# Kernel tuning notes

Hardware: AMD Instinct MI355X
Metric: run time of the kernel (lower is better)

## Reference

```python
import jax, jax.numpy as jnp
import numpy as np

IMG = 416                      # image_shape
DIST = 1075.0                  # isocenter_distance
N_ANG = 320                    # 360 / rotation_resolution(=1.125 deg)
N_DET = IMG                    # detector bins
N_SAMP = IMG                   # integration samples per ray
SCALE = 512.0 / 416.0 * 0.03   # self.scale


def _ray_coords():
    """Pixel-space sample coordinates for every (angle, detector, sample).
    Returns cols, rows of shape [N_ANG, N_DET, N_SAMP] and the step length dt."""
    thetas = (jnp.arange(N_ANG, dtype=jnp.float32) * np.float32(2.0 * np.pi / N_ANG))
    half_diag = (IMG / 2.0) * np.sqrt(2.0)
    gamma_max = np.float32(np.arcsin(half_diag / DIST))  # half fan angle covering image
    gammas = jnp.linspace(-gamma_max, gamma_max, N_DET, dtype=jnp.float32)
    ray_len = np.float32(IMG * np.sqrt(2.0))             # chord length through image
    ts = jnp.linspace(np.float32(DIST - ray_len / 2.0),
                      np.float32(DIST + ray_len / 2.0), N_SAMP, dtype=jnp.float32)
    dt = float(ray_len / (N_SAMP - 1))

    th = thetas[:, None, None]        # [A,1,1]
    gm = gammas[None, :, None]        # [1,D,1]
    t = ts[None, None, :]             # [1,1,S]
    # source position on circle of radius DIST, ray direction toward detector
    sx = np.float32(DIST) * jnp.cos(th)
    sy = np.float32(DIST) * jnp.sin(th)
    x = sx - t * jnp.cos(th + gm)     # [A,D,S] world coords (isocenter at origin)
    y = sy - t * jnp.sin(th + gm)
    ctr = np.float32((IMG - 1) / 2.0)
    return x + ctr, y + ctr, dt       # pixel (col, row) coordinates


def _bilinear(img, cols, rows):
    """Zero-padded bilinear sampling of img[H,W] at float (row,col) coords."""
    c0 = jnp.floor(cols)
    r0 = jnp.floor(rows)
    wc = cols - c0
    wr = rows - r0
    c0i = c0.astype(jnp.int32)
    r0i = r0.astype(jnp.int32)

    def g(ri, ci):
        inb = (ri >= 0) & (ri < IMG) & (ci >= 0) & (ci < IMG)
        v = img[jnp.clip(ri, 0, IMG - 1), jnp.clip(ci, 0, IMG - 1)]
        return jnp.where(inb, v, jnp.float32(0.0))

    return (g(r0i, c0i) * (1 - wr) * (1 - wc)
            + g(r0i, c0i + 1) * (1 - wr) * wc
            + g(r0i + 1, c0i) * wr * (1 - wc)
            + g(r0i + 1, c0i + 1) * wr * wc)


def fan_beam_fp(vol):
    """vol: [B,H,W] -> sinogram [B, N_ANG, N_DET] via ray integration."""
    cols, rows, dt = _ray_coords()
    proj_one = lambda img: _bilinear(img, cols, rows).sum(axis=-1) * jnp.float32(dt)
    return jax.vmap(proj_one)(vol)


def setup_inputs() -> dict:
    key = jax.random.key(0)
    k1, k2 = jax.random.split(key)
    inp = jax.random.normal(k1, (1, 1, IMG, IMG), dtype=jnp.float32)
    tgt = jax.random.normal(k2, (1, 1, IMG, IMG), dtype=jnp.float32)
    return {"input": inp, "target": tgt}


def reference(input, target):
    input_proj = fan_beam_fp(input[:, 0])   # squeeze(1)
    target_proj = fan_beam_fp(target[:, 0])
    return jnp.mean((input_proj - target_proj) ** 2) * jnp.float32(SCALE)
```

## Files before the change

### kernel.cpp

```cpp
#include <hip/hip_runtime.h>
#include <math.h>

#define IMG 416
#define N_ANG 320
#define N_DET 416
#define N_SAMP 416
#define NK (N_SAMP / 8)

#define PSTRIDE 432
#define PROWS   418
#define PBYTES  ((size_t)PROWS * PSTRIDE * 8)

static __device__ __forceinline__ unsigned int f2bf(float f) {
    unsigned int x = __float_as_uint(f);
    return (x + 0x7fffu + ((x >> 16) & 1u)) >> 16;
}

__global__ __launch_bounds__(256) void pack_kernel(const float* __restrict__ a,
                                                   const float* __restrict__ b,
                                                   uint2* __restrict__ P,
                                                   float* __restrict__ out) {
    int i = blockIdx.x * 256 + threadIdx.x;
    if (i == 0) out[0] = 0.0f;
    if (i >= PROWS * PSTRIDE) return;
    int pr = i / PSTRIDE;
    int pc = i - pr * PSTRIDE;
    int r = pr - 1, c = pc - 1;
    float v00 = 0.f, v01 = 0.f, v10 = 0.f, v11 = 0.f;
    bool c0in = (unsigned)c < (unsigned)IMG;
    bool c1in = (unsigned)(c + 1) < (unsigned)IMG;
    if ((unsigned)r < (unsigned)IMG) {
        int base = r * IMG;
        if (c0in) v00 = a[base + c] - b[base + c];
        if (c1in) v01 = a[base + c + 1] - b[base + c + 1];
    }
    if ((unsigned)(r + 1) < (unsigned)IMG) {
        int base = (r + 1) * IMG;
        if (c0in) v10 = a[base + c] - b[base + c];
        if (c1in) v11 = a[base + c + 1] - b[base + c + 1];
    }
    uint2 u;
    u.x = f2bf(v00) | (f2bf(v01) << 16);
    u.y = f2bf(v10) | (f2bf(v11) << 16);
    P[i] = u;
}

__global__ void zero_out_kernel(float* __restrict__ out) {
    if (threadIdx.x == 0) out[0] = 0.0f;
}

__global__ __launch_bounds__(256) void proj_packed(const uint2* __restrict__ P,
                                                   float* __restrict__ out,
                                                   float theta_step, float gmax,
                                                   float gstep, float t0,
                                                   float dtstep, float coef) {
    const int lane = threadIdx.x & 63;
    const int wave = (blockIdx.x * 256 + threadIdx.x) >> 6;
    const int det_base = wave << 3;
    const int a  = det_base / N_DET;
    const int d  = det_base - a * N_DET + (lane >> 3);
    const int s0 = lane & 7;

    const float theta = (float)a * theta_step;
    const float gamma = fmaf((float)d, gstep, -gmax);
    float s1, c1, s2, c2;
    sincosf(theta, &s1, &c1);
    sincosf(theta + gamma, &s2, &c2);
    const float sx = fmaf(1075.0f, c1, 207.5f);
    const float sy = fmaf(1075.0f, s1, 207.5f);

    const float dt8 = 8.0f * dtstep;
    const float tstart = fmaf((float)s0, dtstep, t0);

    const float c2g = (fabsf(c2) < 1e-12f) ? 1e-12f : c2;
    const float s2g = (fabsf(s2) < 1e-12f) ? 1e-12f : s2;
    const float ix = 1.0f / c2g, iy = 1.0f / s2g;
    const float tax = (sx - 416.5f) * ix, tbx = (sx + 1.5f) * ix;
    const float tay = (sy - 416.5f) * iy, tby = (sy + 1.5f) * iy;
    const float t_lo = fmaxf(fminf(tax, tbx), fminf(tay, tby));
    const float t_hi = fminf(fmaxf(tax, tbx), fmaxf(tay, tby));

    const float inv_dt8 = 1.0f / dt8;
    int klo = (int)floorf((t_lo - tstart) * inv_dt8);
    int khi = (int)ceilf((t_hi - tstart) * inv_dt8);
    klo = max(0, min(klo, NK));
    khi = min(NK - 1, khi);

    #pragma unroll
    for (int m = 1; m < 64; m <<= 1) {
        klo = min(klo, __shfl_xor(klo, m, 64));
        khi = max(khi, __shfl_xor(khi, m, 64));
    }
    klo = __builtin_amdgcn_readfirstlane(klo);
    khi = __builtin_amdgcn_readfirstlane(khi);

    const uint2* __restrict__ Pb = P + (PSTRIDE + 1);

    const float tb = fmaf((float)klo, dt8, tstart);
    float col = fmaf(-tb, c2, sx);
    float row = fmaf(-tb, s2, sy);
    const float dcol = -dt8 * c2;
    const float drow = -dt8 * s2;

    float acc = 0.0f;
    #pragma unroll 4
    for (int k = klo; k <= khi; ++k) {
        const float colc = fminf(fmaxf(col, -1.0f), 416.5f);
        const float rowc = fminf(fmaxf(row, -1.0f), 416.5f);
        const int ci = (int)floorf(colc);
        const int ri = (int)floorf(rowc);
        const float wc = colc - (float)ci;
        const float wr = rowc - (float)ri;

        const uint2 u = Pb[ri * PSTRIDE + ci];
        const float v00 = __uint_as_float(u.x << 16);
        const float v01 = __uint_as_float(u.x & 0xffff0000u);
        const float v10 = __uint_as_float(u.y << 16);
        const float v11 = __uint_as_float(u.y & 0xffff0000u);

        const float top = fmaf(wc, v01 - v00, v00);
        const float bot = fmaf(wc, v11 - v10, v10);
        acc = fmaf(wr, bot - top, acc + top);

        col += dcol;
        row += drow;
    }

    #pragma unroll
    for (int m = 1; m < 8; m <<= 1) acc += __shfl_xor(acc, m, 64);
    float sq = acc * acc;
    #pragma unroll
    for (int m = 8; m < 64; m <<= 1) sq += __shfl_xor(sq, m, 64);

    __shared__ float wsum[4];
    if (lane == 0) wsum[threadIdx.x >> 6] = sq;
    __syncthreads();
    if (threadIdx.x == 0)
        atomicAdd(out, (wsum[0] + wsum[1] + wsum[2] + wsum[3]) * coef);
}

__global__ __launch_bounds__(256) void proj_fused(const float* __restrict__ imgA,
                                                  const float* __restrict__ imgB,
                                                  float* __restrict__ out,
                                                  float theta_step, float gmax,
                                                  float gstep, float t0,
                                                  float dtstep, float coef) {
    const int idx = blockIdx.x * 256 + threadIdx.x;
    const int a  = idx / N_DET;
    const int dd = idx - a * N_DET;
    const float theta = (float)a * theta_step;
    const float gamma = fmaf((float)dd, gstep, -gmax);
    float s1, c1, s2, c2;
    sincosf(theta, &s1, &c1);
    sincosf(theta + gamma, &s2, &c2);
    const float sx = 1075.0f * c1 + 207.5f;
    const float sy = 1075.0f * s1 + 207.5f;
    float acc = 0.0f;
    #pragma unroll 4
    for (int s = 0; s < N_SAMP; ++s) {
        const float t   = fmaf((float)s, dtstep, t0);
        const float col = fmaf(-t, c2, sx);
        const float row = fmaf(-t, s2, sy);
        const float c0 = floorf(col);
        const float r0 = floorf(row);
        const float wc = col - c0;
        const float wr = row - r0;
        const int ci = (int)c0;
        const int ri = (int)r0;
        auto G = [&](int r, int c) -> float {
            if ((unsigned)r < (unsigned)IMG && (unsigned)c < (unsigned)IMG)
                return imgA[r * IMG + c] - imgB[r * IMG + c];
            return 0.0f;
        };
        const float v00 = G(ri, ci);
        const float v01 = G(ri, ci + 1);
        const float v10 = G(ri + 1, ci);
        const float v11 = G(ri + 1, ci + 1);
        const float top = fmaf(wc, v01 - v00, v00);
        const float bot = fmaf(wc, v11 - v10, v10);
        acc += fmaf(wr, bot - top, top);
    }
    float sq = acc * acc;
    #pragma unroll
    for (int o = 32; o > 0; o >>= 1) sq += __shfl_down(sq, o, 64);
    __shared__ float wsum[4];
    const int lane = threadIdx.x & 63;
    if (lane == 0) wsum[threadIdx.x >> 6] = sq;
    __syncthreads();
    if (threadIdx.x == 0)
        atomicAdd(out, (wsum[0] + wsum[1] + wsum[2] + wsum[3]) * coef);
}

extern "C" void kernel_launch(void* const* d_in, const int* in_sizes, int n_in,
                              void* d_out, int out_size, void* d_ws, size_t ws_size,
                              hipStream_t stream) {
    const float* in = (const float*)d_in[0];
    const float* tg = (const float*)d_in[1];
    float* out = (float*)d_out;

    const double half_diag = (IMG / 2.0) * sqrt(2.0);
    const double ray_len   = IMG * sqrt(2.0);
    const float  gmax      = (float)asin(half_diag / 1075.0);
    const float  gstep     = (float)(2.0 * (double)gmax / (N_DET - 1));
    const float  t0        = (float)(1075.0 - ray_len / 2.0);
    const float  dtstep    = (float)(ray_len / (N_SAMP - 1));
    const float  theta_step = (float)(2.0 * M_PI / N_ANG);
    const double dt        = ray_len / (N_SAMP - 1);
    const double SCALE     = 512.0 / 416.0 * 0.03;
    const float  coef      = (float)(dt * dt * SCALE / ((double)N_ANG * N_DET));

    const int n_rays = N_ANG * N_DET;
    if (ws_size >= PBYTES) {
        uint2* P = (uint2*)d_ws;
        const int n_ent = PROWS * PSTRIDE;
        pack_kernel<<<(n_ent + 255) / 256, 256, 0, stream>>>(in, tg, P, out);
        proj_packed<<<(n_rays / 8) / 4, 256, 0, stream>>>(
            P, out, theta_step, gmax, gstep, t0, dtstep, coef);
    } else {
        zero_out_kernel<<<1, 64, 0, stream>>>(out);
        proj_fused<<<n_rays / 256, 256, 0, stream>>>(
            in, tg, out, theta_step, gmax, gstep, t0, dtstep, coef);
    }
}
```

Measured before the change: 115.1 us.

## Remap projection work: one wave per sample chunk, lanes across 64 detectors

The projection kernel now uses 512-thread blocks, one block per (angle, group of 64 detectors). Each of the 8 waves integrates one contiguous chunk of 52 samples, and each lane follows one detector ray. Partial sums are combined through shared memory before squaring. Before, each wave covered 8 detectors times 8 interleaved sample offsets. The new layout gives adjacent lanes neighbouring rays at the same depth, which should improve gather locality, and it tightens per-wave loop bounds. The cost is padding lanes (448 slots for 416 detectors) and a block-level sync.

```diff
diff --git a/kernel.cpp b/kernel.cpp
--- a/kernel.cpp
+++ b/kernel.cpp
@@ -5,7 +5,9 @@
 #define N_ANG 320
 #define N_DET 416
 #define N_SAMP 416
-#define NK (N_SAMP / 8)
+#define NCHUNK 8
+#define CHLEN (N_SAMP / NCHUNK)
+#define NGRP 7
 
 #define PSTRIDE 432
 #define PROWS   418
@@ -49,17 +51,19 @@
     if (threadIdx.x == 0) out[0] = 0.0f;
 }
 
-__global__ __launch_bounds__(256) void proj_packed(const uint2* __restrict__ P,
+__global__ __launch_bounds__(512) void proj_packed(const uint2* __restrict__ P,
                                                    float* __restrict__ out,
                                                    float theta_step, float gmax,
                                                    float gstep, float t0,
                                                    float dtstep, float coef) {
-    const int lane = threadIdx.x & 63;
-    const int wave = (blockIdx.x * 256 + threadIdx.x) >> 6;
-    const int det_base = wave << 3;
-    const int a  = det_base / N_DET;
-    const int d  = det_base - a * N_DET + (lane >> 3);
-    const int s0 = lane & 7;
+    const int tid  = threadIdx.x;
+    const int lane = tid & 63;
+    const int wv   = tid >> 6;
+    const int gid  = blockIdx.x;
+    const int a    = gid / NGRP;
+    const int grp  = gid - a * NGRP;
+    const int d    = grp * 64 + lane;
+    const bool valid = (d < N_DET);
 
     const float theta = (float)a * theta_step;
     const float gamma = fmaf((float)d, gstep, -gmax);
@@ -69,9 +73,6 @@
     const float sx = fmaf(1075.0f, c1, 207.5f);
     const float sy = fmaf(1075.0f, s1, 207.5f);
 
-    const float dt8 = 8.0f * dtstep;
-    const float tstart = fmaf((float)s0, dtstep, t0);
-
     const float c2g = (fabsf(c2) < 1e-12f) ? 1e-12f : c2;
     const float s2g = (fabsf(s2) < 1e-12f) ? 1e-12f : s2;
     const float ix = 1.0f / c2g, iy = 1.0f / s2g;
@@ -80,63 +81,69 @@
     const float t_lo = fmaxf(fminf(tax, tbx), fminf(tay, tby));
     const float t_hi = fminf(fmaxf(tax, tbx), fmaxf(tay, tby));
 
-    const float inv_dt8 = 1.0f / dt8;
-    int klo = (int)floorf((t_lo - tstart) * inv_dt8);
-    int khi = (int)ceilf((t_hi - tstart) * inv_dt8);
-    klo = max(0, min(klo, NK));
-    khi = min(NK - 1, khi);
-
+    const float tc0 = fmaf((float)(wv * CHLEN), dtstep, t0);
+    const float inv_dt = 1.0f / dtstep;
+    int jlo = (int)floorf((t_lo - tc0) * inv_dt);
+    int jhi = (int)ceilf((t_hi - tc0) * inv_dt);
+    jlo = max(0, min(jlo, CHLEN));
+    jhi = min(CHLEN - 1, jhi);
+    if (!valid) { jlo = CHLEN; jhi = -1; }
+
+    int ulo = jlo, uhi = jhi;
     #pragma unroll
     for (int m = 1; m < 64; m <<= 1) {
-        klo = min(klo, __shfl_xor(klo, m, 64));
-        khi = max(khi, __shfl_xor(khi, m, 64));
-    }
-    klo = __builtin_amdgcn_readfirstlane(klo);
-    khi = __builtin_amdgcn_readfirstlane(khi);
-
-    const uint2* __restrict__ Pb = P + (PSTRIDE + 1);
-
-    const float tb = fmaf((float)klo, dt8, tstart);
-    float col = fmaf(-tb, c2, sx);
-    float row = fmaf(-tb, s2, sy);
-    const float dcol = -dt8 * c2;
-    const float drow = -dt8 * s2;
+        ulo = min(ulo, __shfl_xor(ulo, m, 64));
+        uhi = max(uhi, __shfl_xor(uhi, m, 64));
+    }
+    ulo = __builtin_amdgcn_readfirstlane(ulo);
+    uhi = __builtin_amdgcn_readfirstlane(uhi);
 
     float acc = 0.0f;
-    #pragma unroll 4
-    for (int k = klo; k <= khi; ++k) {
-        const float colc = fminf(fmaxf(col, -1.0f), 416.5f);
-        const float rowc = fminf(fmaxf(row, -1.0f), 416.5f);
-        const int ci = (int)floorf(colc);
-        const int ri = (int)floorf(rowc);
-        const float wc = colc - (float)ci;
-        const float wr = rowc - (float)ri;
-
-        const uint2 u = Pb[ri * PSTRIDE + ci];
-        const float v00 = __uint_as_float(u.x << 16);
-        const float v01 = __uint_as_float(u.x & 0xffff0000u);
-        const float v10 = __uint_as_float(u.y << 16);
-        const float v11 = __uint_as_float(u.y & 0xffff0000u);
-
-        const float top = fmaf(wc, v01 - v00, v00);
-        const float bot = fmaf(wc, v11 - v10, v10);
-        acc = fmaf(wr, bot - top, acc + top);
-
-        col += dcol;
-        row += drow;
-    }
-
-    #pragma unroll
-    for (int m = 1; m < 8; m <<= 1) acc += __shfl_xor(acc, m, 64);
-    float sq = acc * acc;
-    #pragma unroll
-    for (int m = 8; m < 64; m <<= 1) sq += __shfl_xor(sq, m, 64);
-
-    __shared__ float wsum[4];
-    if (lane == 0) wsum[threadIdx.x >> 6] = sq;
+    if (ulo <= uhi) {
+        const uint2* __restrict__ Pb = P + (PSTRIDE + 1);
+        const float tb = fmaf((float)ulo, dtstep, tc0);
+        float col = fmaf(-tb, c2, sx);
+        float row = fmaf(-tb, s2, sy);
+        const float dcol = -dtstep * c2;
+        const float drow = -dtstep * s2;
+
+        #pragma unroll 4
+        for (int j = ulo; j <= uhi; ++j) {
+            const float colc = fminf(fmaxf(col, -1.0f), 416.5f);
+            const float rowc = fminf(fmaxf(row, -1.0f), 416.5f);
+            const int ci = (int)floorf(colc);
+            const int ri = (int)floorf(rowc);
+            const float wc = colc - (float)ci;
+            const float wr = rowc - (float)ri;
+
+            const uint2 u = Pb[ri * PSTRIDE + ci];
+            const float v00 = __uint_as_float(u.x << 16);
+            const float v01 = __uint_as_float(u.x & 0xffff0000u);
+            const float v10 = __uint_as_float(u.y << 16);
+            const float v11 = __uint_as_float(u.y & 0xffff0000u);
+
+            const float top = fmaf(wc, v01 - v00, v00);
+            const float bot = fmaf(wc, v11 - v10, v10);
+            acc = fmaf(wr, bot - top, acc + top);
+
+            col += dcol;
+            row += drow;
+        }
+    }
+    if (!valid) acc = 0.0f;
+
+    __shared__ float part[NCHUNK][64];
+    part[wv][lane] = acc;
     __syncthreads();
-    if (threadIdx.x == 0)
-        atomicAdd(out, (wsum[0] + wsum[1] + wsum[2] + wsum[3]) * coef);
+    if (tid < 64) {
+        float s = part[0][tid];
+        #pragma unroll
+        for (int w = 1; w < NCHUNK; ++w) s += part[w][tid];
+        float sq = s * s;
+        #pragma unroll
+        for (int m = 1; m < 64; m <<= 1) sq += __shfl_xor(sq, m, 64);
+        if (tid == 0) atomicAdd(out, sq * coef);
+    }
 }
 
 __global__ __launch_bounds__(256) void proj_fused(const float* __restrict__ imgA,
@@ -209,16 +216,15 @@
     const double SCALE     = 512.0 / 416.0 * 0.03;
     const float  coef      = (float)(dt * dt * SCALE / ((double)N_ANG * N_DET));
 
-    const int n_rays = N_ANG * N_DET;
     if (ws_size >= PBYTES) {
         uint2* P = (uint2*)d_ws;
         const int n_ent = PROWS * PSTRIDE;
         pack_kernel<<<(n_ent + 255) / 256, 256, 0, stream>>>(in, tg, P, out);
-        proj_packed<<<(n_rays / 8) / 4, 256, 0, stream>>>(
+        proj_packed<<<N_ANG * NGRP, 512, 0, stream>>>(
             P, out, theta_step, gmax, gstep, t0, dtstep, coef);
     } else {
         zero_out_kernel<<<1, 64, 0, stream>>>(out);
-        proj_fused<<<n_rays / 256, 256, 0, stream>>>(
+        proj_fused<<<(N_ANG * N_DET) / 256, 256, 0, stream>>>(
             in, tg, out, theta_step, gmax, gstep, t0, dtstep, coef);
     }
 }
```

Result: slower. 121.2 us (+5.3%).

## Store packed bilinear quads as FP8 in a 4x4 tiled layout

Applied to the files above, without the earlier changes.

The packed difference-image table changes from two bf16 pairs per texel (8 bytes) to four FP8 values in one 32-bit word, using the hardware pack and unpack conversions. Entries are also laid out in 4x4 texel tiles, so nearby ray samples tend to land in the same cache lines. The aim is to halve the table size and improve cache locality for the gather-bound ray-marching loop. In exchange the sampled values carry only a few mantissa bits, which risks larger error in the final loss.

```diff
diff --git a/kernel.cpp b/kernel.cpp
--- a/kernel.cpp
+++ b/kernel.cpp
@@ -7,24 +7,23 @@
 #define N_SAMP 416
 #define NK (N_SAMP / 8)
 
-#define PSTRIDE 432
-#define PROWS   418
-#define PBYTES  ((size_t)PROWS * PSTRIDE * 8)
-
-static __device__ __forceinline__ unsigned int f2bf(float f) {
-    unsigned int x = __float_as_uint(f);
-    return (x + 0x7fffu + ((x >> 16) & 1u)) >> 16;
-}
+#define TW 105
+#define TABLE_WORDS (TW * TW * 16)
+#define TBYTES ((size_t)TABLE_WORDS * 4)
+
+typedef float vfloat2 __attribute__((ext_vector_type(2)));
 
 __global__ __launch_bounds__(256) void pack_kernel(const float* __restrict__ a,
                                                    const float* __restrict__ b,
-                                                   uint2* __restrict__ P,
+                                                   unsigned int* __restrict__ T,
                                                    float* __restrict__ out) {
     int i = blockIdx.x * 256 + threadIdx.x;
     if (i == 0) out[0] = 0.0f;
-    if (i >= PROWS * PSTRIDE) return;
-    int pr = i / PSTRIDE;
-    int pc = i - pr * PSTRIDE;
+    if (i >= TABLE_WORDS) return;
+    int tile = i >> 4, sub = i & 15;
+    int tr = tile / TW, tc = tile - tr * TW;
+    int pr = tr * 4 + (sub >> 2);
+    int pc = tc * 4 + (sub & 3);
     int r = pr - 1, c = pc - 1;
     float v00 = 0.f, v01 = 0.f, v10 = 0.f, v11 = 0.f;
     bool c0in = (unsigned)c < (unsigned)IMG;
@@ -39,17 +38,16 @@
         if (c0in) v10 = a[base + c] - b[base + c];
         if (c1in) v11 = a[base + c + 1] - b[base + c + 1];
     }
-    uint2 u;
-    u.x = f2bf(v00) | (f2bf(v01) << 16);
-    u.y = f2bf(v10) | (f2bf(v11) << 16);
-    P[i] = u;
+    unsigned int u = __builtin_amdgcn_cvt_pk_fp8_f32(v00, v01, 0u, false);
+    u = __builtin_amdgcn_cvt_pk_fp8_f32(v10, v11, u, true);
+    T[i] = u;
 }
 
 __global__ void zero_out_kernel(float* __restrict__ out) {
     if (threadIdx.x == 0) out[0] = 0.0f;
 }
 
-__global__ __launch_bounds__(256) void proj_packed(const uint2* __restrict__ P,
+__global__ __launch_bounds__(256) void proj_packed(const unsigned int* __restrict__ T,
                                                    float* __restrict__ out,
                                                    float theta_step, float gmax,
                                                    float gstep, float t0,
@@ -94,36 +92,33 @@
     klo = __builtin_amdgcn_readfirstlane(klo);
     khi = __builtin_amdgcn_readfirstlane(khi);
 
-    const uint2* __restrict__ Pb = P + (PSTRIDE + 1);
-
     const float tb = fmaf((float)klo, dt8, tstart);
-    float col = fmaf(-tb, c2, sx);
-    float row = fmaf(-tb, s2, sy);
+    float colp = fmaf(-tb, c2, sx + 1.0f);
+    float rowp = fmaf(-tb, s2, sy + 1.0f);
     const float dcol = -dt8 * c2;
     const float drow = -dt8 * s2;
 
     float acc = 0.0f;
     #pragma unroll 4
     for (int k = klo; k <= khi; ++k) {
-        const float colc = fminf(fmaxf(col, -1.0f), 416.5f);
-        const float rowc = fminf(fmaxf(row, -1.0f), 416.5f);
-        const int ci = (int)floorf(colc);
-        const int ri = (int)floorf(rowc);
-        const float wc = colc - (float)ci;
-        const float wr = rowc - (float)ri;
-
-        const uint2 u = Pb[ri * PSTRIDE + ci];
-        const float v00 = __uint_as_float(u.x << 16);
-        const float v01 = __uint_as_float(u.x & 0xffff0000u);
-        const float v10 = __uint_as_float(u.y << 16);
-        const float v11 = __uint_as_float(u.y & 0xffff0000u);
-
-        const float top = fmaf(wc, v01 - v00, v00);
-        const float bot = fmaf(wc, v11 - v10, v10);
+        const float colc = fminf(fmaxf(colp, 0.0f), 417.5f);
+        const float rowc = fminf(fmaxf(rowp, 0.0f), 417.5f);
+        const int pc = (int)colc;
+        const int pr = (int)rowc;
+        const float wc = colc - (float)pc;
+        const float wr = rowc - (float)pr;
+
+        const int idx = (((pr >> 2) * TW + (pc >> 2)) << 4) + ((pr & 3) << 2) + (pc & 3);
+        const unsigned int u = T[idx];
+        const vfloat2 lo = __builtin_amdgcn_cvt_pk_f32_fp8(u, false);
+        const vfloat2 hi = __builtin_amdgcn_cvt_pk_f32_fp8(u, true);
+
+        const float top = fmaf(wc, lo[1] - lo[0], lo[0]);
+        const float bot = fmaf(wc, hi[1] - hi[0], hi[0]);
         acc = fmaf(wr, bot - top, acc + top);
 
-        col += dcol;
-        row += drow;
+        colp += dcol;
+        rowp += drow;
     }
 
     #pragma unroll
@@ -210,12 +205,11 @@
     const float  coef      = (float)(dt * dt * SCALE / ((double)N_ANG * N_DET));
 
     const int n_rays = N_ANG * N_DET;
-    if (ws_size >= PBYTES) {
-        uint2* P = (uint2*)d_ws;
-        const int n_ent = PROWS * PSTRIDE;
-        pack_kernel<<<(n_ent + 255) / 256, 256, 0, stream>>>(in, tg, P, out);
+    if (ws_size >= TBYTES) {
+        unsigned int* T = (unsigned int*)d_ws;
+        pack_kernel<<<(TABLE_WORDS + 255) / 256, 256, 0, stream>>>(in, tg, T, out);
         proj_packed<<<(n_rays / 8) / 4, 256, 0, stream>>>(
-            P, out, theta_step, gmax, gstep, t0, dtstep, coef);
+            T, out, theta_step, gmax, gstep, t0, dtstep, coef);
     } else {
         zero_out_kernel<<<1, 64, 0, stream>>>(out);
         proj_fused<<<n_rays / 256, 256, 0, stream>>>(
```

Measured after the change: 113.8 us. About the same (-1.1%).
